# Kernel optimization log

Hardware: AMD Instinct MI355X
Metric: run time of the kernel (lower is better)

Reference implementation:

```python
import jax, jax.numpy as jnp
import numpy as np

V, E, H, K, B, T = 50000, 256, 256, 9, 128, 512


def lstm_dir(x, lens, Wih, Whh, b):
    # x: [B,T,E] -> h outputs [B,T,H], packed-sequence semantics:
    # state frozen and outputs zeroed for t >= lens[b].
    Bs, Ts, _ = x.shape
    Hh = Whh.shape[1]
    xw = jnp.einsum('bte,ge->btg', x, Wih) + b  # [B,T,4H] precomputed input proj
    valid = jnp.arange(Ts)[None, :] < lens[:, None]  # [B,T]

    def step(carry, inp):
        h, c = carry
        xw_t, v = inp  # [B,4H], [B]
        gates = xw_t + h @ Whh.T
        i, f, g, o = jnp.split(gates, 4, axis=-1)  # torch gate order i,f,g,o
        i = jax.nn.sigmoid(i)
        f = jax.nn.sigmoid(f)
        g = jnp.tanh(g)
        o = jax.nn.sigmoid(o)
        c_new = f * c + i * g
        h_new = o * jnp.tanh(c_new)
        v = v[:, None]
        return (jnp.where(v, h_new, h), jnp.where(v, c_new, c)), h_new * v

    init = (jnp.zeros((Bs, Hh), x.dtype), jnp.zeros((Bs, Hh), x.dtype))
    _, ys = jax.lax.scan(step, init, (jnp.swapaxes(xw, 0, 1), valid.T))
    return jnp.swapaxes(ys, 0, 1)


def reverse_by_len(x, lens):
    # per-row reversal within valid length; padding stays zero
    Ts = x.shape[1]
    t = jnp.arange(Ts)
    idx = jnp.clip(lens[:, None] - 1 - t[None, :], 0, Ts - 1)
    m = t[None, :] < lens[:, None]
    return jnp.take_along_axis(x, idx[:, :, None], axis=1) * m[:, :, None]


def crf_llh(em, tags, lens, start, end, trans):
    # torchcrf forward with reduction='sum': sum_b (gold score - logZ)
    Bs, Ts, Kk = em.shape
    mask = jnp.arange(Ts)[None, :] < lens[:, None]
    em_t = jnp.take_along_axis(em, tags[..., None], axis=-1)[..., 0]  # [B,T]
    score = start[tags[:, 0]] + em_t[:, 0]
    tr = trans[tags[:, :-1], tags[:, 1:]]  # [B,T-1]
    score = score + jnp.sum((tr + em_t[:, 1:]) * mask[:, 1:], axis=1)
    last_tag = jnp.take_along_axis(tags, (lens - 1)[:, None], axis=1)[:, 0]
    score = score + end[last_tag]

    def step(alpha, inp):
        e_t, m_t = inp  # [B,K], [B]
        nxt = jax.nn.logsumexp(alpha[:, :, None] + trans[None, :, :], axis=1) + e_t
        return jnp.where(m_t[:, None], nxt, alpha), None

    alpha0 = start[None, :] + em[:, 0]  # [B,K]
    alpha, _ = jax.lax.scan(step, alpha0,
                            (jnp.swapaxes(em[:, 1:], 0, 1), mask[:, 1:].T))
    logZ = jax.nn.logsumexp(alpha + end[None, :], axis=1)
    return jnp.sum(score - logZ)


def setup_inputs() -> dict:
    key = jax.random.key(0)
    ks = jax.random.split(key, 16)
    sentences = jax.random.randint(ks[0], (B, T), 0, V)
    tags = jax.random.randint(ks[1], (B, T), 0, K)
    length_list = jax.random.randint(ks[2], (B,), 1, T + 1)  # >=1 so mask[:,0] all true
    s = float(1.0 / np.sqrt(H))
    u = lambda k, sh: jax.random.uniform(k, sh, jnp.float32, -s, s)
    emb = jax.random.normal(ks[3], (V, E), jnp.float32) * float(np.sqrt(2.0 / E))
    return dict(
        sentences=sentences, tags=tags, length_list=length_list,
        emb=emb,
        Wih_f=u(ks[4], (4 * H, E)), Whh_f=u(ks[5], (4 * H, H)), b_f=u(ks[6], (4 * H,)),
        Wih_b=u(ks[7], (4 * H, E)), Whh_b=u(ks[8], (4 * H, H)), b_b=u(ks[9], (4 * H,)),
        W_out=u(ks[10], (K, 2 * H)), b_out=u(ks[11], (K,)),
        start=jax.random.uniform(ks[12], (K,), jnp.float32, -0.1, 0.1),
        end=jax.random.uniform(ks[13], (K,), jnp.float32, -0.1, 0.1),
        trans=jax.random.uniform(ks[14], (K, K), jnp.float32, -0.1, 0.1),
    )


def reference(sentences, tags, length_list, emb, Wih_f, Whh_f, b_f,
              Wih_b, Whh_b, b_b, W_out, b_out, start, end, trans):
    x = emb[sentences]  # [B,T,E]
    h_f = lstm_dir(x, length_list, Wih_f, Whh_f, b_f)
    x_rev = reverse_by_len(x, length_list)
    h_b = reverse_by_len(lstm_dir(x_rev, length_list, Wih_b, Whh_b, b_b), length_list)
    hcat = jnp.concatenate([h_f, h_b], axis=-1)  # [B,T,2H]
    # Dropout is identity in eval mode
    em = jnp.einsum('bth,kh->btk', hcat, W_out) + b_out  # [B,T,K]
    return crf_llh(em, tags, length_list, start, end, trans)
```

## Files before the change

kernel.cpp:

```cpp
#include <hip/hip_runtime.h>
#include <hip/hip_bf16.h>

typedef short v8s __attribute__((ext_vector_type(8)));
typedef int   v8i __attribute__((ext_vector_type(8)));
typedef float v4f __attribute__((ext_vector_type(4)));
typedef float v2f __attribute__((ext_vector_type(2)));

#define T_ 512

template<int HI>
__device__ __forceinline__ v2f cvt2(unsigned int wsrc){
  return __builtin_amdgcn_cvt_pk_f32_fp8((int)wsrc, HI);
}
__device__ __forceinline__ v2f rcp2(v2f d){
  return (v2f){__builtin_amdgcn_rcpf(d.x), __builtin_amdgcn_rcpf(d.y)};
}
__device__ __forceinline__ v2f tanh2(v2f x){
  v2f x2 = x*x;
  v2f num = x*(x2 + 27.f);
  v2f den = x2*9.f + 27.f;
  v2f r = num * rcp2(den);
  return (v2f){__builtin_amdgcn_fmed3f(r.x,-1.f,1.f),
               __builtin_amdgcn_fmed3f(r.y,-1.f,1.f)};
}
__device__ __forceinline__ v2f sigm2(v2f x){
  v2f x2 = x*x;
  v2f num = x*(x2 + 108.f);
  v2f den = x2*36.f + 432.f;
  v2f r = num * rcp2(den);
  v2f rc = (v2f){__builtin_amdgcn_fmed3f(r.x,-0.5f,0.5f),
                 __builtin_amdgcn_fmed3f(r.y,-0.5f,0.5f)};
  return rc + 0.5f;
}
__device__ __forceinline__ int pi_col(int p){
  return ((p>>5)<<5) + ((p&1)<<4) + ((p&31)>>1);
}
__device__ __forceinline__ v8i ld32(const void* p){
  uint4 lo = *(const uint4*)p;
  uint4 hi = *(const uint4*)((const char*)p + 16);
  v8i r;
  r[0]=(int)lo.x; r[1]=(int)lo.y; r[2]=(int)lo.z; r[3]=(int)lo.w;
  r[4]=(int)hi.x; r[5]=(int)hi.y; r[6]=(int)hi.z; r[7]=(int)hi.w;
  return r;
}
__device__ __forceinline__ unsigned f2fp4(float x){
  unsigned s = (x < 0.f) ? 8u : 0u;
  float a = fabsf(x);
  unsigned m;
  if      (a < 0.25f) m=0u; else if (a < 0.75f) m=1u;
  else if (a < 1.25f) m=2u; else if (a < 1.75f) m=3u;
  else if (a < 2.5f ) m=4u; else if (a < 3.5f ) m=5u;
  else if (a < 5.f  ) m=6u; else m=7u;
  return s|m;
}
__device__ __forceinline__ unsigned pk8(float a, float b, float c, float d){
  int w = __builtin_amdgcn_cvt_pk_fp8_f32(a, b, 0, 0);
  w     = __builtin_amdgcn_cvt_pk_fp8_f32(c, d, w, 1);
  return (unsigned)w;
}
__device__ __forceinline__ unsigned enc4(v2f h){
  v2f t = h*4.f;
  unsigned b = 0;
  #pragma unroll
  for (int s=0;s<2;++s){
    float v = s ? t.y : t.x;
    float ax = __builtin_amdgcn_fmed3f(fabsf(v), 0.f, 4.f);
    float gl = fmaf(ax, 2.f, 12582912.f);
    float gh = ax + 12582912.f;
    unsigned ql = __builtin_bit_cast(unsigned, gl) & 7u;
    unsigned qh = (__builtin_bit_cast(unsigned, gh) & 7u) + 2u;
    unsigned c  = (ax > 1.75f) ? qh : ql;
    unsigned sg = (__builtin_bit_cast(unsigned, v) >> 28) & 8u;
    b |= (c | sg) << (4*s);
  }
  return b;
}

__global__ __launch_bounds__(256) void prep_k(
    const float* __restrict__ WihA, const float* __restrict__ WihB,
    const float* __restrict__ WhhF, const float* __restrict__ WhhB,
    unsigned char* __restrict__ wih_out, unsigned char* __restrict__ whh_out)
{
  int blk = blockIdx.x;
  if (blk < 64){
    int idx = blk*256 + threadIdx.x;
    int lane = idx & 63;
    int t2 = idx >> 6;
    int ntile = t2 & 127;
    int kt = t2 >> 7;
    int n = ntile*16 + (lane&15);
    const float* W = (n < 1024) ? (WihA + (size_t)n*256) : (WihB + (size_t)(n-1024)*256);
    int k0 = kt*128 + (lane>>4)*32;
    unsigned words[8];
    #pragma unroll
    for (int e=0;e<8;++e)
      words[e] = pk8(W[k0+e*4], W[k0+e*4+1], W[k0+e*4+2], W[k0+e*4+3]);
    unsigned char* d = wih_out + (size_t)idx*32;
    *(uint4*)(d)      = make_uint4(words[0], words[1], words[2], words[3]);
    *(uint4*)(d + 16) = make_uint4(words[4], words[5], words[6], words[7]);
  } else {
    int idx = (blk-64)*256 + threadIdx.x;
    int lane = idx & 63;
    int t2 = idx >> 6;
    int ntile = t2 & 63;
    int kt = (t2>>6) & 1;
    int dir = t2 >> 7;
    const float* W = dir ? WhhB : WhhF;
    int n = ntile*16 + (lane&15);
    int kbase = kt*128 + (lane>>4)*32;
    const float* row = W + (size_t)n*256;
    unsigned words[4];
    #pragma unroll
    for (int d4=0;d4<4;++d4){
      unsigned acc = 0;
      #pragma unroll
      for (int j=0;j<8;++j){
        float v = row[pi_col(kbase + d4*8 + j)] * 64.f;
        acc |= f2fp4(v) << (4*j);
      }
      words[d4] = acc;
    }
    *(uint4*)(whh_out + (size_t)idx*16) = make_uint4(words[0], words[1], words[2], words[3]);
  }
}

__global__ __launch_bounds__(256) void xw_gemm_k(
    const int* __restrict__ sent, const float* __restrict__ emb,
    const unsigned char* __restrict__ wihg, const int* __restrict__ lens,
    const float* __restrict__ bfv, const float* __restrict__ bbv,
    unsigned char* __restrict__ xw)
{
  int mt = blockIdx.x;
  if (((mt&3)<<7) >= lens[mt>>2]) return;
  __shared__ unsigned char A[128][272];
  int tid = threadIdx.x;
  {
    int row = tid>>1, half = tid&1;
    int tok = sent[mt*128 + row];
    const float4* s = (const float4*)(emb + (size_t)tok*256 + half*128);
    unsigned char* drow = &A[row][half*128];
    #pragma unroll
    for (int c4=0; c4<8; ++c4){
      unsigned w0[4];
      #pragma unroll
      for (int u=0; u<4; ++u){
        float4 v = s[c4*4+u];
        w0[u] = pk8(v.x, v.y, v.z, v.w);
      }
      *(uint4*)(drow + c4*16) = make_uint4(w0[0], w0[1], w0[2], w0[3]);
    }
  }
  __syncthreads();
  int w = tid>>6, lane = tid&63, lr = lane&15, lq = lane>>4;
  #pragma unroll 1
  for (int i4=0; i4<4; ++i4){
    int dnv = w*4 + i4;
    int dn = dnv>>3, v = dnv&7;
    const float* bb = dn ? bbv : bfv;
    float bias[8];
    #pragma unroll
    for (int e=0;e<8;++e){
      int q = e>>1, s = e&1;
      bias[e] = bb[q*256 + v*32 + s*16 + lr];
    }
    #pragma unroll 1
    for (int mh=0; mh<2; ++mh){
      v4f acc[8][4];
      #pragma unroll
      for (int e=0;e<8;++e)
        #pragma unroll
        for (int mm=0;mm<4;++mm) acc[e][mm] = (v4f){0.f,0.f,0.f,0.f};
      #pragma unroll
      for (int kt=0;kt<2;++kt){
        v8i a0 = ld32(&A[mh*64 +  0 + lr][kt*128 + lq*32]);
        v8i a1 = ld32(&A[mh*64 + 16 + lr][kt*128 + lq*32]);
        v8i a2 = ld32(&A[mh*64 + 32 + lr][kt*128 + lq*32]);
        v8i a3 = ld32(&A[mh*64 + 48 + lr][kt*128 + lq*32]);
        #pragma unroll
        for (int e=0;e<8;++e){
          int q = e>>1, s = e&1;
          int ntile = dn*64 + q*16 + v*2 + s;
          v8i bfr = ld32(wihg + ((size_t)(kt*128 + ntile)*64 + lane)*32);
          acc[e][0] = __builtin_amdgcn_mfma_scale_f32_16x16x128_f8f6f4(
                        a0, bfr, acc[e][0], 0,0, 0,0x7f7f7f7f, 0,0x7f7f7f7f);
          acc[e][1] = __builtin_amdgcn_mfma_scale_f32_16x16x128_f8f6f4(
                        a1, bfr, acc[e][1], 0,0, 0,0x7f7f7f7f, 0,0x7f7f7f7f);
          acc[e][2] = __builtin_amdgcn_mfma_scale_f32_16x16x128_f8f6f4(
                        a2, bfr, acc[e][2], 0,0, 0,0x7f7f7f7f, 0,0x7f7f7f7f);
          acc[e][3] = __builtin_amdgcn_mfma_scale_f32_16x16x128_f8f6f4(
                        a3, bfr, acc[e][3], 0,0, 0,0x7f7f7f7f, 0,0x7f7f7f7f);
        }
      }
      #pragma unroll
      for (int mm=0;mm<4;++mm){
        #pragma unroll
        for (int j=0;j<4;++j){
          int row = mt*128 + mh*64 + mm*16 + lq*4 + j;
          unsigned lo = pk8(acc[0][mm][j]+bias[0], acc[1][mm][j]+bias[1],
                            acc[2][mm][j]+bias[2], acc[3][mm][j]+bias[3]);
          unsigned hi = pk8(acc[4][mm][j]+bias[4], acc[5][mm][j]+bias[5],
                            acc[6][mm][j]+bias[6], acc[7][mm][j]+bias[7]);
          *(uint2*)(xw + ((size_t)dn*65536 + row)*1024 + v*128 + lr*8)
              = make_uint2(lo, hi);
        }
      }
    }
  }
}

__global__ __launch_bounds__(512,1) void lstm_k(
    const unsigned char* __restrict__ xw,
    const unsigned char* __restrict__ whh4,
    const int* __restrict__ lens,
    unsigned char* __restrict__ hout)
{
  int bid = blockIdx.x, dir = bid>>5, grp = bid&31;
  int tid = threadIdx.x, w = tid>>6, lane = tid&63, lr = lane&15, lq = lane>>4;
  int wu = __builtin_amdgcn_readfirstlane(w);
  __shared__ unsigned char hbuf[2][16][136];
  __shared__ int tmax_s;
  for (int i=tid*4; i<2*16*136; i+=512*4) *(unsigned int*)(&((unsigned char*)hbuf)[i]) = 0u;
  if (tid==0){
    int mx=0;
    for (int i=0;i<4;++i){ int l = lens[grp*4+i]; mx = l>mx? l:mx; }
    tmax_s = mx;
  }
  v8i wreg[16];
  const unsigned char* wb = whh4 + (size_t)dir*131072 + (size_t)lane*16;
  #pragma unroll
  for (int kt=0;kt<2;++kt){
    #pragma unroll
    for (int nt=0;nt<8;++nt){
      int ntile = (nt>>1)*16 + wu*2 + (nt&1);
      uint4 t = *(const uint4*)(wb + (size_t)(kt*64 + ntile)*1024);
      v8i r;
      r[0]=(int)t.x; r[1]=(int)t.y; r[2]=(int)t.z; r[3]=(int)t.w;
      r[4]=0; r[5]=0; r[6]=0; r[7]=0;
      wreg[kt*8+nt] = r;
    }
  }
  #pragma unroll
  for (int i=0;i<16;++i) asm volatile("" : "+v"(wreg[i]));
  int seq = grp*4 + lq;
  int ln = lens[seq];
  v2f cc = (v2f){0.f, 0.f};
  const size_t dbase = (size_t)dir*65536;
  const unsigned char* xbase = xw + (dbase + (size_t)seq*T_)*1024 + wu*128 + lr*8;
  unsigned char* hbase = hout + (dbase + (size_t)seq*T_)*256 + wu*32 + lr*2;
  unsigned char* lw0 = &hbuf[1][lq*4][wu*16 + lr];
  unsigned char* lw1 = &hbuf[0][lq*4][wu*16 + lr];
  const unsigned char* lr0 = &hbuf[0][lr][lq*16];
  const unsigned char* lr1 = &hbuf[1][lr][lq*16];
  __syncthreads();
  int tmax = tmax_s;
  uint2 xv = *(const uint2*)(xbase + (size_t)(dir ? (ln-1) : 0)*1024);

  #define STEP_BODY(TE_EXPR, POS_EXPR)                                         \
    int cur = t&1;                                                             \
    int tn = (t+1<tmax)? t+1 : t;                                              \
    int te = (TE_EXPR);                                                        \
    uint2 xn = *(const uint2*)(xbase + ((size_t)te<<10));                      \
    const unsigned char* lrd = cur? lr1 : lr0;                                 \
    v2f xi = cvt2<0>(xv.x), xf = cvt2<1>(xv.x);                                \
    v2f xg = cvt2<0>(xv.y), xo = cvt2<1>(xv.y);                                \
    v4f acc[8];                                                                \
    _Pragma("unroll")                                                          \
    for (int nt=0;nt<8;++nt) asm("" : "=v"(acc[nt]));                          \
    acc[0][0] = xi.x; acc[1][0] = xi.y;                                        \
    acc[2][0] = xf.x; acc[3][0] = xf.y;                                        \
    acc[4][0] = xg.x; acc[5][0] = xg.y;                                        \
    acc[6][0] = xo.x; acc[7][0] = xo.y;                                        \
    _Pragma("unroll")                                                          \
    for (int kt=0;kt<2;++kt){                                                  \
      uint4 hh = *(const uint4*)(lrd + kt*64);                                 \
      v8i a;                                                                   \
      a[0]=(int)hh.x; a[1]=(int)hh.y; a[2]=(int)hh.z; a[3]=(int)hh.w;          \
      a[4]=0; a[5]=0; a[6]=0; a[7]=0;                                          \
      _Pragma("unroll")                                                        \
      for (int nt=0;nt<8;++nt)                                                 \
        acc[nt] = __builtin_amdgcn_mfma_scale_f32_16x16x128_f8f6f4(            \
                    a, wreg[kt*8+nt], acc[nt], 4, 4,                           \
                    0, 0x7D7D7D7D, 0, 0x79797979);                             \
    }                                                                          \
    int pos = (POS_EXPR);                                                      \
    v2f gi = (v2f){acc[0][0], acc[1][0]};                                      \
    v2f gf = (v2f){acc[2][0], acc[3][0]};                                      \
    v2f gg = (v2f){acc[4][0], acc[5][0]};                                      \
    v2f go = (v2f){acc[6][0], acc[7][0]};                                      \
    v2f iv = sigm2(gi), fv = sigm2(gf), gv = tanh2(gg), ov = sigm2(go);        \
    v2f cn = fv*cc + iv*gv;                                                    \
    v2f hn = ov*tanh2(cn);                                                     \
    cc = cn;                                                                   \
    *(cur? lw1 : lw0) = (unsigned char)enc4(hn);                               \
    int hp = __builtin_amdgcn_cvt_pk_fp8_f32(hn.x, hn.y, 0, 0);                \
    *(unsigned short*)(hbase + ((size_t)pos<<8)) = (unsigned short)(hp&0xffff);\
    xv = xn;                                                                   \
    asm volatile("s_waitcnt lgkmcnt(0)" ::: "memory");                         \
    __builtin_amdgcn_s_barrier();                                              \
    __builtin_amdgcn_sched_barrier(0);

  if (dir == 0){
    for (int t=0; t<tmax; ++t){
      STEP_BODY(tn, t)
    }
  } else {
    for (int t=0; t<tmax; ++t){
      STEP_BODY((tn<ln)? (ln-1-tn) : tn, (t<ln)? (ln-1-t) : t)
    }
  }
  #undef STEP_BODY
}

__global__ __launch_bounds__(256) void em_k(
    const unsigned char* __restrict__ hout,
    const float* __restrict__ Wout, const float* __restrict__ bout,
    const int* __restrict__ lens,
    float* __restrict__ em)
{
  __shared__ float Ws[9*512];
  for (int i=threadIdx.x;i<9*512;i+=256){
    int k = i>>9, p = i&511;
    int d = p>>8, pp = p&255;
    Ws[i] = Wout[k*512 + d*256 + pi_col(pp)];
  }
  __syncthreads();
  int wv = blockIdx.x*4 + (threadIdx.x>>6);
  int lane = threadIdx.x & 63;
  int g = lane>>4, r = lane&15;
  int m = wv*4 + g;
  const unsigned char* hf = hout + (size_t)m*256 + r*16;
  const unsigned char* hb = hout + ((size_t)65536 + m)*256 + r*16;
  uint4 vf = *(const uint4*)hf;
  uint4 vb = *(const uint4*)hb;
  float xf[16], xb[16];
  {
    v2f d0=cvt2<0>(vf.x), d1=cvt2<1>(vf.x), d2=cvt2<0>(vf.y), d3=cvt2<1>(vf.y);
    v2f d4=cvt2<0>(vf.z), d5=cvt2<1>(vf.z), d6=cvt2<0>(vf.w), d7=cvt2<1>(vf.w);
    xf[0]=d0.x; xf[1]=d0.y; xf[2]=d1.x; xf[3]=d1.y;
    xf[4]=d2.x; xf[5]=d2.y; xf[6]=d3.x; xf[7]=d3.y;
    xf[8]=d4.x; xf[9]=d4.y; xf[10]=d5.x; xf[11]=d5.y;
    xf[12]=d6.x; xf[13]=d6.y; xf[14]=d7.x; xf[15]=d7.y;
  }
  {
    v2f d0=cvt2<0>(vb.x), d1=cvt2<1>(vb.x), d2=cvt2<0>(vb.y), d3=cvt2<1>(vb.y);
    v2f d4=cvt2<0>(vb.z), d5=cvt2<1>(vb.z), d6=cvt2<0>(vb.w), d7=cvt2<1>(vb.w);
    xb[0]=d0.x; xb[1]=d0.y; xb[2]=d1.x; xb[3]=d1.y;
    xb[4]=d2.x; xb[5]=d2.y; xb[6]=d3.x; xb[7]=d3.y;
    xb[8]=d4.x; xb[9]=d4.y; xb[10]=d5.x; xb[11]=d5.y;
    xb[12]=d6.x; xb[13]=d6.y; xb[14]=d7.x; xb[15]=d7.y;
  }
  float a[9];
  #pragma unroll
  for (int k=0;k<9;++k){
    float s = 0.f;
    #pragma unroll
    for (int e=0;e<16;++e)
      s += xf[e]*Ws[k*512 + r*16 + e] + xb[e]*Ws[k*512 + 256 + r*16 + e];
    a[k]=s;
  }
  #pragma unroll
  for (int k=0;k<9;++k){
    #pragma unroll
    for (int off=8; off; off>>=1) a[k] += __shfl_xor(a[k], off, 64);
  }
  int b = m>>9, t = m&511;
  if (r==0 && t < lens[b]){
    float* d = em + (size_t)m*9;
    #pragma unroll
    for (int k=0;k<9;++k) d[k] = a[k] + bout[k];
  }
}

__global__ __launch_bounds__(256) void crf_k(
    const float* __restrict__ em, const int* __restrict__ tags,
    const int* __restrict__ lens, const float* __restrict__ startv,
    const float* __restrict__ endv, const float* __restrict__ trans,
    float* __restrict__ out)
{
  int wid = blockIdx.x*4 + (threadIdx.x>>6);
  int lane = threadIdx.x & 63;
  const float* e = em + (size_t)wid*T_*9;
  const int* tg = tags + (size_t)wid*T_;
  int L = lens[wid];
  float p = 0.f;
  for (int t = 1+lane; t < L; t += 64)
    p += trans[tg[t-1]*9 + tg[t]] + e[(size_t)t*9 + tg[t]];
  if (lane==0) p += startv[tg[0]] + e[tg[0]] + endv[tg[L-1]];
  #pragma unroll
  for (int off=32; off; off>>=1) p += __shfl_xor(p, off, 64);
  float tcol[9];
  #pragma unroll
  for (int i=0;i<9;++i) tcol[i] = (lane<9) ? trans[i*9 + lane] : 0.f;
  float alpha = (lane<9) ? (startv[lane] + e[lane]) : -1e30f;
  for (int t=1; t<L; ++t){
    float vs[9]; float mx = -1e30f;
    #pragma unroll
    for (int i=0;i<9;++i){
      float ai = __shfl(alpha, i, 64);
      vs[i] = ai + tcol[i];
      mx = fmaxf(mx, vs[i]);
    }
    float s = 0.f;
    #pragma unroll
    for (int i=0;i<9;++i) s += __expf(vs[i]-mx);
    float na = mx + __logf(s) + ((lane<9)? e[(size_t)t*9+lane] : 0.f);
    alpha = (lane<9) ? na : -1e30f;
  }
  float v = (lane<9) ? (alpha + endv[lane]) : -1e30f;
  float mx = v;
  #pragma unroll
  for (int off=32; off; off>>=1) mx = fmaxf(mx, __shfl_xor(mx, off, 64));
  float s = __expf(v-mx);
  #pragma unroll
  for (int off=32; off; off>>=1) s += __shfl_xor(s, off, 64);
  float logZ = mx + __logf(s);
  if (lane==0) atomicAdd(out, p - logZ);
}

extern "C" void kernel_launch(void* const* d_in, const int* in_sizes, int n_in,
                              void* d_out, int out_size, void* d_ws, size_t ws_size,
                              hipStream_t stream)
{
  const int*   sent  = (const int*)d_in[0];
  const int*   tags  = (const int*)d_in[1];
  const int*   lens  = (const int*)d_in[2];
  const float* emb   = (const float*)d_in[3];
  const float* Wih_f = (const float*)d_in[4];
  const float* Whh_f = (const float*)d_in[5];
  const float* b_f   = (const float*)d_in[6];
  const float* Wih_b = (const float*)d_in[7];
  const float* Whh_b = (const float*)d_in[8];
  const float* b_b   = (const float*)d_in[9];
  const float* Wout  = (const float*)d_in[10];
  const float* bout  = (const float*)d_in[11];
  const float* startv= (const float*)d_in[12];
  const float* endv  = (const float*)d_in[13];
  const float* trans = (const float*)d_in[14];
  char* ws = (char*)d_ws;
  unsigned char* wihg8 = (unsigned char*)(ws);
  unsigned char* whh4  = (unsigned char*)(ws + (size_t)524288);
  unsigned char* xw    = (unsigned char*)(ws + (size_t)1048576);
  unsigned char* hout  = (unsigned char*)(ws + (size_t)135266304);
  float* em            = (float*)(ws + (size_t)168820736);
  float* outp = (float*)d_out;

  (void)hipMemsetAsync(outp, 0, sizeof(float), stream);
  prep_k<<<128, 256, 0, stream>>>(Wih_f, Wih_b, Whh_f, Whh_b, wihg8, whh4);
  xw_gemm_k<<<512, 256, 0, stream>>>(sent, emb, wihg8, lens, b_f, b_b, xw);
  lstm_k<<<64, 512, 0, stream>>>(xw, whh4, lens, hout);
  em_k<<<4096, 256, 0, stream>>>(hout, Wout, bout, lens, em);
  crf_k<<<32, 256, 0, stream>>>(em, tags, lens, startv, endv, trans, outp);
}
```

Measured before the change: 721.6 us.

## Merge forward and backward LSTM directions into one 1024-thread block per group

The LSTM recurrence kernel now runs both directions of the same 4-sequence group inside one 1024-thread block: waves 0-7 handle forward, waves 8-15 backward, each with its own shared h buffer. The grid shrinks from 64 to 32 blocks, and a single barrier per step synchronizes both directions. The direction is now chosen at runtime per wave, the macro specialization is removed, and so is the asm pin on the weight registers. This may help per-step latency by sharing one workgroup across both directions, but it risks the slower direction stalling the other at each barrier, extra branch cost, and register pressure at 1024 threads.

```diff
diff --git a/kernel.cpp b/kernel.cpp
--- a/kernel.cpp
+++ b/kernel.cpp
@@ -208,30 +208,31 @@
   }
 }
 
-__global__ __launch_bounds__(512,1) void lstm_k(
+__global__ __launch_bounds__(1024,1) void lstm_k(
     const unsigned char* __restrict__ xw,
     const unsigned char* __restrict__ whh4,
     const int* __restrict__ lens,
     unsigned char* __restrict__ hout)
 {
-  int bid = blockIdx.x, dir = bid>>5, grp = bid&31;
+  int grp = blockIdx.x;
   int tid = threadIdx.x, w = tid>>6, lane = tid&63, lr = lane&15, lq = lane>>4;
-  int wu = __builtin_amdgcn_readfirstlane(w);
-  __shared__ unsigned char hbuf[2][16][136];
+  int dirw = w>>3, w8 = w&7;
+  __shared__ unsigned char hbuf[2][2][16][136];
   __shared__ int tmax_s;
-  for (int i=tid*4; i<2*16*136; i+=512*4) *(unsigned int*)(&((unsigned char*)hbuf)[i]) = 0u;
+  for (int i=tid*4; i<2*2*16*136; i+=1024*4)
+    *(unsigned int*)(&((unsigned char*)hbuf)[i]) = 0u;
   if (tid==0){
     int mx=0;
     for (int i=0;i<4;++i){ int l = lens[grp*4+i]; mx = l>mx? l:mx; }
     tmax_s = mx;
   }
   v8i wreg[16];
-  const unsigned char* wb = whh4 + (size_t)dir*131072 + (size_t)lane*16;
+  const unsigned char* wb = whh4 + (size_t)dirw*131072 + (size_t)lane*16;
   #pragma unroll
   for (int kt=0;kt<2;++kt){
     #pragma unroll
     for (int nt=0;nt<8;++nt){
-      int ntile = (nt>>1)*16 + wu*2 + (nt&1);
+      int ntile = (nt>>1)*16 + w8*2 + (nt&1);
       uint4 t = *(const uint4*)(wb + (size_t)(kt*64 + ntile)*1024);
       v8i r;
       r[0]=(int)t.x; r[1]=(int)t.y; r[2]=(int)t.z; r[3]=(int)t.w;
@@ -239,76 +240,63 @@
       wreg[kt*8+nt] = r;
     }
   }
-  #pragma unroll
-  for (int i=0;i<16;++i) asm volatile("" : "+v"(wreg[i]));
   int seq = grp*4 + lq;
   int ln = lens[seq];
   v2f cc = (v2f){0.f, 0.f};
-  const size_t dbase = (size_t)dir*65536;
-  const unsigned char* xbase = xw + (dbase + (size_t)seq*T_)*1024 + wu*128 + lr*8;
-  unsigned char* hbase = hout + (dbase + (size_t)seq*T_)*256 + wu*32 + lr*2;
-  unsigned char* lw0 = &hbuf[1][lq*4][wu*16 + lr];
-  unsigned char* lw1 = &hbuf[0][lq*4][wu*16 + lr];
-  const unsigned char* lr0 = &hbuf[0][lr][lq*16];
-  const unsigned char* lr1 = &hbuf[1][lr][lq*16];
+  const size_t dbase = (size_t)dirw*65536;
+  const unsigned char* xbase = xw + (dbase + (size_t)seq*T_)*1024 + w8*128 + lr*8;
+  unsigned char* hbase = hout + (dbase + (size_t)seq*T_)*256 + w8*32 + lr*2;
+  unsigned char* lw0 = &hbuf[1][dirw][lq*4][w8*16 + lr];
+  unsigned char* lw1 = &hbuf[0][dirw][lq*4][w8*16 + lr];
+  const unsigned char* lr0 = &hbuf[0][dirw][lr][lq*16];
+  const unsigned char* lr1 = &hbuf[1][dirw][lr][lq*16];
   __syncthreads();
   int tmax = tmax_s;
-  uint2 xv = *(const uint2*)(xbase + (size_t)(dir ? (ln-1) : 0)*1024);
-
-  #define STEP_BODY(TE_EXPR, POS_EXPR)                                         \
-    int cur = t&1;                                                             \
-    int tn = (t+1<tmax)? t+1 : t;                                              \
-    int te = (TE_EXPR);                                                        \
-    uint2 xn = *(const uint2*)(xbase + ((size_t)te<<10));                      \
-    const unsigned char* lrd = cur? lr1 : lr0;                                 \
-    v2f xi = cvt2<0>(xv.x), xf = cvt2<1>(xv.x);                                \
-    v2f xg = cvt2<0>(xv.y), xo = cvt2<1>(xv.y);                                \
-    v4f acc[8];                                                                \
-    _Pragma("unroll")                                                          \
-    for (int nt=0;nt<8;++nt) asm("" : "=v"(acc[nt]));                          \
-    acc[0][0] = xi.x; acc[1][0] = xi.y;                                        \
-    acc[2][0] = xf.x; acc[3][0] = xf.y;                                        \
-    acc[4][0] = xg.x; acc[5][0] = xg.y;                                        \
-    acc[6][0] = xo.x; acc[7][0] = xo.y;                                        \
-    _Pragma("unroll")                                                          \
-    for (int kt=0;kt<2;++kt){                                                  \
-      uint4 hh = *(const uint4*)(lrd + kt*64);                                 \
-      v8i a;                                                                   \
-      a[0]=(int)hh.x; a[1]=(int)hh.y; a[2]=(int)hh.z; a[3]=(int)hh.w;          \
-      a[4]=0; a[5]=0; a[6]=0; a[7]=0;                                          \
-      _Pragma("unroll")                                                        \
-      for (int nt=0;nt<8;++nt)                                                 \
-        acc[nt] = __builtin_amdgcn_mfma_scale_f32_16x16x128_f8f6f4(            \
-                    a, wreg[kt*8+nt], acc[nt], 4, 4,                           \
-                    0, 0x7D7D7D7D, 0, 0x79797979);                             \
-    }                                                                          \
-    int pos = (POS_EXPR);                                                      \
-    v2f gi = (v2f){acc[0][0], acc[1][0]};                                      \
-    v2f gf = (v2f){acc[2][0], acc[3][0]};                                      \
-    v2f gg = (v2f){acc[4][0], acc[5][0]};                                      \
-    v2f go = (v2f){acc[6][0], acc[7][0]};                                      \
-    v2f iv = sigm2(gi), fv = sigm2(gf), gv = tanh2(gg), ov = sigm2(go);        \
-    v2f cn = fv*cc + iv*gv;                                                    \
-    v2f hn = ov*tanh2(cn);                                                     \
-    cc = cn;                                                                   \
-    *(cur? lw1 : lw0) = (unsigned char)enc4(hn);                               \
-    int hp = __builtin_amdgcn_cvt_pk_fp8_f32(hn.x, hn.y, 0, 0);                \
-    *(unsigned short*)(hbase + ((size_t)pos<<8)) = (unsigned short)(hp&0xffff);\
-    xv = xn;                                                                   \
-    asm volatile("s_waitcnt lgkmcnt(0)" ::: "memory");                         \
-    __builtin_amdgcn_s_barrier();                                              \
+  uint2 xv = *(const uint2*)(xbase + (size_t)(dirw ? (ln-1) : 0)*1024);
+  for (int t=0; t<tmax; ++t){
+    int cur = t&1;
+    int tn = (t+1<tmax)? t+1 : t;
+    int te = dirw ? ((tn<ln)? (ln-1-tn) : tn) : tn;
+    uint2 xn = *(const uint2*)(xbase + ((size_t)te<<10));
+    const unsigned char* lrd = cur? lr1 : lr0;
+    v2f xi = cvt2<0>(xv.x), xf = cvt2<1>(xv.x);
+    v2f xg = cvt2<0>(xv.y), xo = cvt2<1>(xv.y);
+    v4f acc[8];
+    #pragma unroll
+    for (int nt=0;nt<8;++nt) asm("" : "=v"(acc[nt]));
+    acc[0][0] = xi.x; acc[1][0] = xi.y;
+    acc[2][0] = xf.x; acc[3][0] = xf.y;
+    acc[4][0] = xg.x; acc[5][0] = xg.y;
+    acc[6][0] = xo.x; acc[7][0] = xo.y;
+    #pragma unroll
+    for (int kt=0;kt<2;++kt){
+      uint4 hh = *(const uint4*)(lrd + kt*64);
+      v8i a;
+      a[0]=(int)hh.x; a[1]=(int)hh.y; a[2]=(int)hh.z; a[3]=(int)hh.w;
+      a[4]=0; a[5]=0; a[6]=0; a[7]=0;
+      #pragma unroll
+      for (int nt=0;nt<8;++nt)
+        acc[nt] = __builtin_amdgcn_mfma_scale_f32_16x16x128_f8f6f4(
+                    a, wreg[kt*8+nt], acc[nt], 4, 4,
+                    0, 0x7D7D7D7D, 0, 0x79797979);
+    }
+    int pos = dirw ? ((t<ln)? (ln-1-t) : t) : t;
+    v2f gi = (v2f){acc[0][0], acc[1][0]};
+    v2f gf = (v2f){acc[2][0], acc[3][0]};
+    v2f gg = (v2f){acc[4][0], acc[5][0]};
+    v2f go = (v2f){acc[6][0], acc[7][0]};
+    v2f iv = sigm2(gi), fv = sigm2(gf), gv = tanh2(gg), ov = sigm2(go);
+    v2f cn = fv*cc + iv*gv;
+    v2f hn = ov*tanh2(cn);
+    cc = cn;
+    *(cur? lw1 : lw0) = (unsigned char)enc4(hn);
+    int hp = __builtin_amdgcn_cvt_pk_fp8_f32(hn.x, hn.y, 0, 0);
+    *(unsigned short*)(hbase + ((size_t)pos<<8)) = (unsigned short)(hp&0xffff);
+    xv = xn;
+    asm volatile("s_waitcnt lgkmcnt(0)" ::: "memory");
+    __builtin_amdgcn_s_barrier();
     __builtin_amdgcn_sched_barrier(0);
-
-  if (dir == 0){
-    for (int t=0; t<tmax; ++t){
-      STEP_BODY(tn, t)
-    }
-  } else {
-    for (int t=0; t<tmax; ++t){
-      STEP_BODY((tn<ln)? (ln-1-tn) : tn, (t<ln)? (ln-1-t) : t)
-    }
-  }
-  #undef STEP_BODY
+  }
 }
 
 __global__ __launch_bounds__(256) void em_k(
@@ -447,7 +435,7 @@
   (void)hipMemsetAsync(outp, 0, sizeof(float), stream);
   prep_k<<<128, 256, 0, stream>>>(Wih_f, Wih_b, Whh_f, Whh_b, wihg8, whh4);
   xw_gemm_k<<<512, 256, 0, stream>>>(sent, emb, wihg8, lens, b_f, b_b, xw);
-  lstm_k<<<64, 512, 0, stream>>>(xw, whh4, lens, hout);
+  lstm_k<<<32, 1024, 0, stream>>>(xw, whh4, lens, hout);
   em_k<<<4096, 256, 0, stream>>>(hout, Wout, bout, lens, em);
   crf_k<<<32, 256, 0, stream>>>(em, tags, lens, startv, endv, trans, outp);
 }
```

Result: slower. 1.387 ms (+92.2%).
